# Kernel optimization log

Measured on AMD Instinct MI355X. Metric: run time of the kernel, lower is better.

The kernel has to match this reference:

```python
import jax, jax.numpy as jnp
import numpy as np

N, Q, C, T = 32, 300, 92, 32  # batch, queries, classes, targets-per-image
L_CLS, L_IOU, L_L1 = 1.0, 2.0, 5.0


def _cxcywh_to_xyxy(b):
    cx, cy, w, h = b[..., 0], b[..., 1], b[..., 2], b[..., 3]
    return jnp.stack([cx - 0.5 * w, cy - 0.5 * h, cx + 0.5 * w, cy + 0.5 * h], axis=-1)


def _generalized_box_iou(a, b):
    # a: [P,4] xyxy, b: [M,4] xyxy -> [P,M]
    area_a = (a[:, 2] - a[:, 0]) * (a[:, 3] - a[:, 1])
    area_b = (b[:, 2] - b[:, 0]) * (b[:, 3] - b[:, 1])
    lt = jnp.maximum(a[:, None, :2], b[None, :, :2])
    rb = jnp.minimum(a[:, None, 2:], b[None, :, 2:])
    wh = jnp.clip(rb - lt, 0.0)
    inter = wh[..., 0] * wh[..., 1]
    union = area_a[:, None] + area_b[None, :] - inter
    iou = inter / union
    lt_c = jnp.minimum(a[:, None, :2], b[None, :, :2])
    rb_c = jnp.maximum(a[:, None, 2:], b[None, :, 2:])
    wh_c = jnp.clip(rb_c - lt_c, 0.0)
    area_c = wh_c[..., 0] * wh_c[..., 1]
    return iou - (area_c - union) / area_c


def _cost_matrix(pred_logits, pred_boxes, tgt_labels, tgt_boxes):
    out_prob = jax.nn.softmax(pred_logits.reshape(-1, C), axis=-1)  # [N*Q, C]
    out_bbox = pred_boxes.reshape(-1, 4)                            # [N*Q, 4]
    cost_class = -out_prob[:, tgt_labels]                           # [N*Q, N*T]
    cost_bbox = jnp.sum(jnp.abs(out_bbox[:, None, :] - tgt_boxes[None, :, :]), axis=-1)
    cost_giou = -_generalized_box_iou(_cxcywh_to_xyxy(out_bbox), _cxcywh_to_xyxy(tgt_boxes))
    cost = L_L1 * cost_bbox + L_CLS * cost_class + L_IOU * cost_giou
    return cost.reshape(N, Q, N * T)


def _lsa(cost):
    # Jonker-Volgenant shortest augmenting path (e-maxx), cost: [n, m], n <= m.
    # Returns col4row: for each row, the assigned column.
    n, m = cost.shape
    INF = np.inf
    u = np.zeros(n + 1)
    v = np.zeros(m + 1)
    p = np.zeros(m + 1, dtype=np.int64)   # p[j] = row assigned to column j (1-based)
    way = np.zeros(m + 1, dtype=np.int64)
    for i in range(1, n + 1):
        p[0] = i
        j0 = 0
        minv = np.full(m + 1, INF)
        used = np.zeros(m + 1, dtype=bool)
        while True:
            used[j0] = True
            i0 = p[j0]
            free = ~used[1:]
            cur = cost[i0 - 1] - u[i0] - v[1:]
            upd = free & (cur < minv[1:])
            minv[1:][upd] = cur[upd]
            way[1:][upd] = j0
            j1 = 1 + int(np.argmin(np.where(free, minv[1:], INF)))
            delta = minv[j1]
            used_idx = np.nonzero(used)[0]
            u[p[used_idx]] += delta
            v[used_idx] -= delta
            minv[1:][free] -= delta
            j0 = j1
            if p[j0] == 0:
                break
        while j0:
            j1 = way[j0]
            p[j0] = p[j1]
            j0 = j1
    ans = np.full(n, -1, dtype=np.int64)
    js = np.nonzero(p[1:])[0]
    ans[p[1:][js] - 1] = js
    return ans


def _multiplier(cost):
    c_np = np.asarray(jax.device_get(cost))  # [N, Q, N*T]
    mult = np.zeros_like(c_np)
    for i in range(N):
        block = c_np[i, :, i * T:(i + 1) * T]  # [Q, T], sample i's own targets
        q_of_t = _lsa(block.T)                 # for each target, matched query
        # NOTE: faithfully replicates the original code's `count = 0` reset,
        # so columns are indexed locally (first T columns of the global axis).
        mult[i, q_of_t, np.arange(T)] = 1.0
    return jnp.asarray(mult)


def setup_inputs() -> dict:
    key = jax.random.key(0)
    k1, k2, k3, k4 = jax.random.split(key, 4)
    return {
        "pred_logits": jax.random.normal(k1, (N, Q, C), dtype=jnp.float32),
        "pred_boxes": jax.random.uniform(k2, (N, Q, 4), dtype=jnp.float32),
        "tgt_labels": jax.random.randint(k3, (N * T,), 0, C, dtype=jnp.int64),
        "tgt_boxes": jax.random.uniform(k4, (N * T, 4), dtype=jnp.float32),
    }


def reference(pred_logits, pred_boxes, tgt_labels, tgt_boxes):
    cost = _cost_matrix(pred_logits, pred_boxes, tgt_labels, tgt_boxes)
    mult = _multiplier(cost)
    return jnp.sum(cost * mult)
```

## Files before the change

### kernel.cpp

```cpp
#include <hip/hip_runtime.h>
#include <cfloat>
#include <cmath>

#define Nn 32
#define Qq 300
#define Cc 92
#define Tt 32
#define KCOLS 5
#define LSTRIDE 93
#define GSZ 10
#define GCOLS 30
#define AUCTION_ROUNDS 10
#define AUCTION_EPS 1e-3f

__device__ inline float wave_min_bcast(float x) {
#define DPPMIN(ctrl) { int _t = __builtin_amdgcn_update_dpp( \
        __float_as_int(x), __float_as_int(x), ctrl, 0xf, 0xf, false); \
        x = fminf(x, __int_as_float(_t)); }
    DPPMIN(0x111) DPPMIN(0x112) DPPMIN(0x114) DPPMIN(0x118)
    DPPMIN(0x142) DPPMIN(0x143)
#undef DPPMIN
    return __int_as_float(__builtin_amdgcn_readlane(__float_as_int(x), 63));
}

__device__ inline int sel5i(const int a[KCOLS], int k) {
    int r = a[0];
    if (k == 1) r = a[1];
    if (k == 2) r = a[2];
    if (k == 3) r = a[3];
    if (k == 4) r = a[4];
    return r;
}

__device__ inline float readlane_f(float v, int lane) {
    return __int_as_float(__builtin_amdgcn_readlane(__float_as_int(v), lane));
}

__device__ inline void softmax_lds(const float* __restrict__ srow,
                                   float& mx, float& inv_s) {
    float m0 = -FLT_MAX, m1 = -FLT_MAX, m2 = -FLT_MAX, m3 = -FLT_MAX;
#pragma unroll
    for (int c = 0; c < Cc; c += 4) {
        m0 = fmaxf(m0, srow[c + 0]);
        m1 = fmaxf(m1, srow[c + 1]);
        m2 = fmaxf(m2, srow[c + 2]);
        m3 = fmaxf(m3, srow[c + 3]);
    }
    const float m = fmaxf(fmaxf(m0, m1), fmaxf(m2, m3));
    float s0 = 0.f, s1 = 0.f, s2 = 0.f, s3 = 0.f;
#pragma unroll
    for (int c = 0; c < Cc; c += 4) {
        s0 += __expf(srow[c + 0] - m);
        s1 += __expf(srow[c + 1] - m);
        s2 += __expf(srow[c + 2] - m);
        s3 += __expf(srow[c + 3] - m);
    }
    mx = m; inv_s = 1.f / ((s0 + s1) + (s2 + s3));
}

__device__ inline float det_cost(float cx, float cy, float w, float h,
                                 float bcx, float bcy, float bw, float bh,
                                 float cls) {
    const float ax0 = cx - 0.5f * w, ay0 = cy - 0.5f * h;
    const float ax1 = cx + 0.5f * w, ay1 = cy + 0.5f * h;
    const float areaA = (ax1 - ax0) * (ay1 - ay0);

    const float l1 = fabsf(cx - bcx) + fabsf(cy - bcy) +
                     fabsf(w - bw) + fabsf(h - bh);

    const float bx0 = bcx - 0.5f * bw, by0 = bcy - 0.5f * bh;
    const float bx1 = bcx + 0.5f * bw, by1 = bcy + 0.5f * bh;
    const float areaB = (bx1 - bx0) * (by1 - by0);

    const float ltx = fmaxf(ax0, bx0), lty = fmaxf(ay0, by0);
    const float rbx = fminf(ax1, bx1), rby = fminf(ay1, by1);
    const float iw = fmaxf(rbx - ltx, 0.f), ih = fmaxf(rby - lty, 0.f);
    const float inter = iw * ih;
    const float uni = areaA + areaB - inter;
    const float iou = inter / uni;

    const float ex0 = fminf(ax0, bx0), ey0 = fminf(ay0, by0);
    const float ex1 = fmaxf(ax1, bx1), ey1 = fmaxf(ay1, by1);
    const float areaC = fmaxf(ex1 - ex0, 0.f) * fmaxf(ey1 - ey0, 0.f);
    const float giou = iou - (areaC - uni) / areaC;

    return 5.f * l1 + cls - 2.f * giou;
}

__global__ __launch_bounds__(320) void fused_kernel(
    const float* __restrict__ logits,
    const float* __restrict__ pboxes,
    const int*   __restrict__ tlabels,
    const float* __restrict__ tboxes,
    float* __restrict__ out)
{
    const int b = blockIdx.x;
    const int tid = threadIdx.x;

    extern __shared__ float s_lg[];
    __shared__ float s_diag[Tt * Qq];
    __shared__ float s_tb[Tt * 4];
    __shared__ int   s_tl[Tt];
    __shared__ int   pairs[Tt];
    __shared__ float s_v[Qq];
    __shared__ float s_u[Tt + 1];
    __shared__ int   s_colrow[Qq];
    __shared__ unsigned long long s_bid64[Qq];
    __shared__ float s_pm1[320], s_pm2[320];
    __shared__ int   s_pa[320];
    __shared__ unsigned s_mask;

    if (tid < Tt * 4) s_tb[tid] = tboxes[b * Tt * 4 + tid];
    if (tid < Tt)     s_tl[tid] = tlabels[b * Tt + tid];
    if (tid < Qq)     { s_v[tid] = 0.f; s_colrow[tid] = 0; }
    if (tid == 0)     s_mask = 0xffffffffu;

    {
        const float4* lgb = reinterpret_cast<const float4*>(
            logits + (size_t)b * Qq * Cc);
#pragma unroll 4
        for (int g = tid; g < Qq * 23; g += 320) {
            const float4 v = lgb[g];
            const int r = g / 23, c4 = (g - r * 23) * 4;
            float* dst = &s_lg[r * LSTRIDE + c4];
            dst[0] = v.x; dst[1] = v.y; dst[2] = v.z; dst[3] = v.w;
        }
    }
    __syncthreads();

    if (tid < Qq) {
        const float* srow = &s_lg[tid * LSTRIDE];
        float mx, inv_s;
        softmax_lds(srow, mx, inv_s);
        const float4 pbv = reinterpret_cast<const float4*>(pboxes)[b * Qq + tid];
#pragma unroll 4
        for (int t = 0; t < Tt; ++t) {
            const float cls = -__expf(srow[s_tl[t]] - mx) * inv_s;
            s_diag[t * Qq + tid] =
                det_cost(pbv.x, pbv.y, pbv.z, pbv.w,
                         s_tb[t * 4 + 0], s_tb[t * 4 + 1],
                         s_tb[t * 4 + 2], s_tb[t * 4 + 3], cls);
        }
    }
    __syncthreads();

    {
        const int grp = tid / GSZ;
        const int g   = tid - grp * GSZ;
        for (int round = 0; round < AUCTION_ROUNDS; ++round) {
            const unsigned msk = s_mask;
            if (msk == 0) break;
            for (int j = tid; j < Qq; j += 320) s_bid64[j] = 0ull;

            if (msk & (1u << grp)) {
                const float* rowp = &s_diag[grp * Qq];
                float m1 = INFINITY, m2 = INFINITY; int a1 = 0;
                const int c0 = g * GCOLS;
#pragma unroll
                for (int j = 0; j < GCOLS; ++j) {
                    const int cidx = c0 + j;
                    const float c = rowp[cidx] - s_v[cidx];
                    if (c < m1) { m2 = m1; m1 = c; a1 = cidx + 1; }
                    else if (c < m2) m2 = c;
                }
                s_pm1[tid] = m1; s_pm2[tid] = m2; s_pa[tid] = a1;
            }
            __syncthreads();

            float g1 = 0.f, g2 = 0.f; int j1 = 0;
            unsigned long long mypk = 0ull;
            if (tid < Tt && (msk & (1u << tid))) {
                float best = INFINITY, second = INFINITY, bm2 = INFINITY;
                int ba = 0;
                const int base = tid * GSZ;
#pragma unroll
                for (int q = 0; q < GSZ; ++q) {
                    const float v = s_pm1[base + q];
                    if (v < best) {
                        second = best; best = v;
                        ba = s_pa[base + q]; bm2 = s_pm2[base + q];
                    } else if (v < second) second = v;
                }
                g1 = best; g2 = fminf(second, bm2); j1 = ba;
                mypk = ((unsigned long long)(__float_as_uint(g2 - g1) + 1u) << 32)
                       | (unsigned)(0xffffffffu - (unsigned)(tid + 1));
                atomicMax(&s_bid64[j1 - 1], mypk);
            }
            __syncthreads();

            if (tid < Tt && (msk & (1u << tid))) {
                const int row = tid + 1;
                const float eps = (round < 2) ? 0.f : AUCTION_EPS;
                if (s_bid64[j1 - 1] == mypk) {
                    const int old = s_colrow[j1 - 1];
                    s_colrow[j1 - 1] = row;
                    s_v[j1 - 1] -= (g2 - g1) + eps;
                    s_u[row] = g2;
                    atomicAnd(&s_mask, ~(1u << tid));
                    if (old) atomicOr(&s_mask, 1u << (old - 1));
                } else {
                    s_u[row] = g1;
                }
            }
            __syncthreads();
        }
    }

    if (tid >= 64) return;
    const int lane = tid;
    const bool inval4 = (lane + 256) >= Qq;

    float u_reg = (lane >= 1 && lane <= Tt) ? s_u[lane] : 0.f;
    float v_r[KCOLS]; int p_r[KCOLS];
#pragma unroll
    for (int k = 0; k < KCOLS; ++k) {
        const int j = lane + 64 * k;
        v_r[k] = (j < Qq) ? s_v[j] : 0.f;
        p_r[k] = (j < Qq) ? s_colrow[j] : 0;
    }

    for (unsigned rem = s_mask; rem; rem &= rem - 1) {
        const int i = __ffs(rem);

        float minv_r[KCOLS], vmask[KCOLS], am[KCOLS];
        int way_r[KCOLS];
#pragma unroll
        for (int k = 0; k < KCOLS; ++k) {
            minv_r[k] = FLT_MAX; way_r[k] = 0;
            const bool inv = (k == 4) && inval4;
            vmask[k] = inv ? -INFINITY : v_r[k];
            am[k]    = inv ?  INFINITY : 0.f;
        }
        float markg = 0.f;
        int   ent = 0;
        int   j0 = 0, i0 = i;
        float du = 0.f - readlane_f(u_reg, i);
        int   jfinal = 0;
        float Dfinal = 0.f;

        const float* rowp = &s_diag[(i0 - 1) * Qq + lane];
        float c0 = rowp[0], c1 = rowp[64], c2 = rowp[128], c3 = rowp[192],
              c4 = rowp[256];

        while (true) {
            const float cc[KCOLS] = {c0, c1, c2, c3, c4};
            float sv[KCOLS];
#pragma unroll
            for (int k = 0; k < KCOLS; ++k) {
                const float cur = (cc[k] + du) - vmask[k];
                const bool lt = cur < minv_r[k];
                way_r[k]  = lt ? j0  : way_r[k];
                minv_r[k] = lt ? cur : minv_r[k];
                sv[k] = minv_r[k] + am[k];
            }
            float val = sv[0];
            int   kb  = 0;
#pragma unroll
            for (int k = 1; k < KCOLS; ++k)
                if (sv[k] < val) { val = sv[k]; kb = k; }

            const float gmin = wave_min_bcast(val);
            const unsigned long long mask = __ballot(val == gmin);
            const int src = __ffsll((long long)mask) - 1;
            const int colid = lane + 1 + (kb << 6);
            const int pk = (sel5i(p_r, kb) << 16) | colid;
            const int got = __builtin_amdgcn_readlane(pk, src);
            const int j1   = got & 0xffff;
            const int rowm = got >> 16;

            const int k1 = (j1 - 1) >> 6;
            const bool own = (lane == ((j1 - 1) & 63));
#pragma unroll
            for (int k = 0; k < KCOLS; ++k)
                if (own && k == k1) { vmask[k] = -INFINITY; am[k] = INFINITY; }

            if (rowm == 0) { jfinal = j1; Dfinal = gmin; break; }

            i0 = rowm; j0 = j1;
            rowp = &s_diag[(i0 - 1) * Qq + lane];
            c0 = rowp[0]; c1 = rowp[64]; c2 = rowp[128]; c3 = rowp[192];
            c4 = rowp[256];
            du = gmin - readlane_f(u_reg, i0);
            markg = (lane == rowm) ? gmin : markg;
            ent   = (lane == rowm) ? 1    : ent;
        }

#pragma unroll
        for (int k = 0; k < KCOLS; ++k) {
            bool usedk = (am[k] == INFINITY);
            if (k == 4) usedk = usedk && !inval4;
            v_r[k] -= usedk ? (Dfinal - minv_r[k]) : 0.f;
        }
        u_reg += (lane == i) ? Dfinal : (ent ? (Dfinal - markg) : 0.f);

        int jj = jfinal;
        while (jj) {
            const int ow = (jj - 1) & 63, kk = (jj - 1) >> 6;
            const int jprev = __builtin_amdgcn_readlane(sel5i(way_r, kk), ow);
            int pnew;
            if (jprev == 0) pnew = i;
            else pnew = __builtin_amdgcn_readlane(sel5i(p_r, (jprev - 1) >> 6),
                                                  (jprev - 1) & 63);
            const bool own = (lane == ow);
#pragma unroll
            for (int k = 0; k < KCOLS; ++k) if (own && k == kk) p_r[k] = pnew;
            jj = jprev;
        }
    }

#pragma unroll
    for (int k = 0; k < KCOLS; ++k)
        if (p_r[k]) pairs[p_r[k] - 1] = lane + 64 * k;
    __threadfence_block();

    float part = 0.f;
    if (lane < Tt) {
        const int q = pairs[lane];
        const float* srow = &s_lg[q * LSTRIDE];
        float mx, inv_s;
        softmax_lds(srow, mx, inv_s);
        const float4 pbv = reinterpret_cast<const float4*>(pboxes)[b * Qq + q];
        const float4 tbv = reinterpret_cast<const float4*>(tboxes)[lane];
        const float cls = -__expf(srow[tlabels[lane]] - mx) * inv_s;
        part = det_cost(pbv.x, pbv.y, pbv.z, pbv.w,
                        tbv.x, tbv.y, tbv.z, tbv.w, cls);
    }
    for (int off = 32; off > 0; off >>= 1) part += __shfl_down(part, off);
    if (lane == 0) atomicAdd(out, part);
}

extern "C" void kernel_launch(void* const* d_in, const int* in_sizes, int n_in,
                              void* d_out, int out_size, void* d_ws, size_t ws_size,
                              hipStream_t stream) {
    const float* logits  = (const float*)d_in[0];
    const float* pboxes  = (const float*)d_in[1];
    const int*   tlabels = (const int*)d_in[2];
    const float* tboxes  = (const float*)d_in[3];
    float* out = (float*)d_out;

    (void)hipMemsetAsync(out, 0, sizeof(float), stream);
    const size_t lg_bytes = (size_t)Qq * LSTRIDE * sizeof(float);
    fused_kernel<<<Nn, 320, lg_bytes, stream>>>(logits, pboxes, tlabels, tboxes, out);
}
```

Baseline: 86.21 us.

## Widen block to 1024 threads and parallelise cost-matrix build over all entries

Raises the block size from 320 to 1024 threads. The per-target cost matrix is now built by spreading all T×Q entries across every thread, instead of each of 300 threads looping over 32 targets. The softmax max and inverse-sum are stored in shared memory so the final cost evaluation reuses them rather than recomputing the softmax. The auction phase is guarded to the first 320 threads. Extra waves add barrier cost and may lower occupancy, and any hidden code that assumes 320 threads could misbehave.

Measured after the change: 80.22 us. 6.9% less time.

```diff
diff --git a/kernel.cpp b/kernel.cpp
--- a/kernel.cpp
+++ b/kernel.cpp
@@ -12,6 +12,7 @@
 #define GCOLS 30
 #define AUCTION_ROUNDS 10
 #define AUCTION_EPS 1e-3f
+#define NTHREADS 1024
 
 __device__ inline float wave_min_bcast(float x) {
 #define DPPMIN(ctrl) { int _t = __builtin_amdgcn_update_dpp( \
@@ -87,7 +88,7 @@
     return 5.f * l1 + cls - 2.f * giou;
 }
 
-__global__ __launch_bounds__(320) void fused_kernel(
+__global__ __launch_bounds__(NTHREADS) void fused_kernel(
     const float* __restrict__ logits,
     const float* __restrict__ pboxes,
     const int*   __restrict__ tlabels,
@@ -102,6 +103,7 @@
     __shared__ float s_tb[Tt * 4];
     __shared__ int   s_tl[Tt];
     __shared__ int   pairs[Tt];
+    __shared__ float2 s_mxis[Qq];
     __shared__ float s_v[Qq];
     __shared__ float s_u[Tt + 1];
     __shared__ int   s_colrow[Qq];
@@ -119,7 +121,7 @@
         const float4* lgb = reinterpret_cast<const float4*>(
             logits + (size_t)b * Qq * Cc);
 #pragma unroll 4
-        for (int g = tid; g < Qq * 23; g += 320) {
+        for (int g = tid; g < Qq * 23; g += NTHREADS) {
             const float4 v = lgb[g];
             const int r = g / 23, c4 = (g - r * 23) * 4;
             float* dst = &s_lg[r * LSTRIDE + c4];
@@ -129,18 +131,21 @@
     __syncthreads();
 
     if (tid < Qq) {
-        const float* srow = &s_lg[tid * LSTRIDE];
         float mx, inv_s;
-        softmax_lds(srow, mx, inv_s);
-        const float4 pbv = reinterpret_cast<const float4*>(pboxes)[b * Qq + tid];
-#pragma unroll 4
-        for (int t = 0; t < Tt; ++t) {
-            const float cls = -__expf(srow[s_tl[t]] - mx) * inv_s;
-            s_diag[t * Qq + tid] =
-                det_cost(pbv.x, pbv.y, pbv.z, pbv.w,
-                         s_tb[t * 4 + 0], s_tb[t * 4 + 1],
-                         s_tb[t * 4 + 2], s_tb[t * 4 + 3], cls);
-        }
+        softmax_lds(&s_lg[tid * LSTRIDE], mx, inv_s);
+        s_mxis[tid] = make_float2(mx, inv_s);
+    }
+    __syncthreads();
+
+    for (int e = tid; e < Tt * Qq; e += NTHREADS) {
+        const int t = e / Qq, q = e - t * Qq;
+        const float2 mi = s_mxis[q];
+        const float* srow = &s_lg[q * LSTRIDE];
+        const float cls = -__expf(srow[s_tl[t]] - mi.x) * mi.y;
+        const float4 pbv = reinterpret_cast<const float4*>(pboxes)[b * Qq + q];
+        s_diag[e] = det_cost(pbv.x, pbv.y, pbv.z, pbv.w,
+                             s_tb[t * 4 + 0], s_tb[t * 4 + 1],
+                             s_tb[t * 4 + 2], s_tb[t * 4 + 3], cls);
     }
     __syncthreads();
 
@@ -150,9 +155,9 @@
         for (int round = 0; round < AUCTION_ROUNDS; ++round) {
             const unsigned msk = s_mask;
             if (msk == 0) break;
-            for (int j = tid; j < Qq; j += 320) s_bid64[j] = 0ull;
-
-            if (msk & (1u << grp)) {
+            for (int j = tid; j < Qq; j += NTHREADS) s_bid64[j] = 0ull;
+
+            if (tid < 320 && (msk & (1u << grp))) {
                 const float* rowp = &s_diag[grp * Qq];
                 float m1 = INFINITY, m2 = INFINITY; int a1 = 0;
                 const int c0 = g * GCOLS;
@@ -316,12 +321,11 @@
     float part = 0.f;
     if (lane < Tt) {
         const int q = pairs[lane];
+        const float2 mi = s_mxis[q];
         const float* srow = &s_lg[q * LSTRIDE];
-        float mx, inv_s;
-        softmax_lds(srow, mx, inv_s);
+        const float cls = -__expf(srow[tlabels[lane]] - mi.x) * mi.y;
         const float4 pbv = reinterpret_cast<const float4*>(pboxes)[b * Qq + q];
         const float4 tbv = reinterpret_cast<const float4*>(tboxes)[lane];
-        const float cls = -__expf(srow[tlabels[lane]] - mx) * inv_s;
         part = det_cost(pbv.x, pbv.y, pbv.z, pbv.w,
                         tbv.x, tbv.y, tbv.z, tbv.w, cls);
     }
@@ -340,5 +344,6 @@
 
     (void)hipMemsetAsync(out, 0, sizeof(float), stream);
     const size_t lg_bytes = (size_t)Qq * LSTRIDE * sizeof(float);
-    fused_kernel<<<Nn, 320, lg_bytes, stream>>>(logits, pboxes, tlabels, tboxes, out);
-}
+    fused_kernel<<<Nn, NTHREADS, lg_bytes, stream>>>(logits, pboxes, tlabels,
+                                                     tboxes, out);
+}
```
